# Kernel optimization log

Hardware: AMD Instinct MI355X
Metric: run time of the kernel (lower is better)

Reference implementation:

```python
import jax, jax.numpy as jnp
import numpy as np

B, S, E, H, L, D, G, V = 32, 256, 300, 256, 4000, 256, 512, 50000
LIN1, LIN2 = 512, 256  # linear_size


def _glorot(key, shape):
    fan_in, fan_out = shape[-1], shape[-2] if len(shape) > 1 else shape[-1]
    std = np.sqrt(2.0 / (fan_in + fan_out))
    return jax.random.normal(key, shape, dtype=jnp.float32) * std


def setup_inputs() -> dict:
    key = jax.random.key(0)
    ks = jax.random.split(key, 20)
    tokens = jax.random.randint(ks[0], (B, S), 1, V)  # avoid padding_idx=0
    emb_table = jax.random.normal(ks[1], (V, E), dtype=jnp.float32) * 0.1
    emb_table = emb_table.at[0].set(0.0)  # padding row
    # bidirectional LSTM (1 layer), torch gate order i,f,g,o
    w_ih_f = _glorot(ks[2], (4 * H, E));  w_hh_f = _glorot(ks[3], (4 * H, H))
    b_f = jnp.zeros((4 * H,), jnp.float32)
    w_ih_b = _glorot(ks[4], (4 * H, E));  w_hh_b = _glorot(ks[5], (4 * H, H))
    b_b = jnp.zeros((4 * H,), jnp.float32)
    # MLAttention: Linear(2H -> L, bias=False)
    attn_w = _glorot(ks[6], (L, 2 * H))
    # label graph branch
    label_emb = _glorot(ks[7], (L, D))
    adj_raw = (jax.random.uniform(ks[8], (L, L)) < 0.004).astype(jnp.float32)
    adj_raw = adj_raw + jnp.eye(L, dtype=jnp.float32)
    deg = jnp.sum(adj_raw, axis=1, keepdims=True)
    adj = adj_raw / deg  # row-normalized dense adjacency [L, L]
    gcn_w = _glorot(ks[9], (D, G));  gcn_b = jnp.zeros((G,), jnp.float32)
    # MLLinear([2H+G, 512, 256], 1)
    w1 = _glorot(ks[10], (2 * H + G, LIN1));  b1 = jnp.zeros((LIN1,), jnp.float32)
    w2 = _glorot(ks[11], (LIN1, LIN2));       b2 = jnp.zeros((LIN2,), jnp.float32)
    w_out = _glorot(ks[12], (LIN2, 1));       b_out = jnp.zeros((1,), jnp.float32)
    return dict(tokens=tokens, emb_table=emb_table,
                w_ih_f=w_ih_f, w_hh_f=w_hh_f, b_f=b_f,
                w_ih_b=w_ih_b, w_hh_b=w_hh_b, b_b=b_b,
                attn_w=attn_w, label_emb=label_emb, adj=adj,
                gcn_w=gcn_w, gcn_b=gcn_b,
                w1=w1, b1=b1, w2=w2, b2=b2, w_out=w_out, b_out=b_out)


def _lstm_dir(x_gates, w_hh, reverse):
    # x_gates: [B, S, 4H] precomputed input projections (+bias)
    def step(carry, xt):
        h, c = carry
        gates = xt + h @ w_hh.T
        i, f, g, o = jnp.split(gates, 4, axis=-1)
        c = jax.nn.sigmoid(f) * c + jax.nn.sigmoid(i) * jnp.tanh(g)
        h = jax.nn.sigmoid(o) * jnp.tanh(c)
        return (h, c), h
    b = x_gates.shape[0]
    init = (jnp.zeros((b, H), x_gates.dtype), jnp.zeros((b, H), x_gates.dtype))
    _, hs = jax.lax.scan(step, init, jnp.swapaxes(x_gates, 0, 1), reverse=reverse)
    return jnp.swapaxes(hs, 0, 1)  # [B, S, H]


def reference(tokens, emb_table, w_ih_f, w_hh_f, b_f, w_ih_b, w_hh_b, b_b,
              attn_w, label_emb, adj, gcn_w, gcn_b,
              w1, b1, w2, b2, w_out, b_out):
    masks = tokens != 0  # [B, S]
    emb_out = emb_table[tokens]  # [B, S, E]
    # bidirectional LSTM -> [B, S, 2H]
    gates_f = jnp.einsum('bse,ge->bsg', emb_out, w_ih_f) + b_f
    gates_b = jnp.einsum('bse,ge->bsg', emb_out, w_ih_b) + b_b
    rnn_out = jnp.concatenate([_lstm_dir(gates_f, w_hh_f, False),
                               _lstm_dir(gates_b, w_hh_b, True)], axis=-1)
    # MLAttention: per-label attention over sequence
    scores = jnp.einsum('bsh,lh->bls', rnn_out, attn_w)  # [B, L, S]
    scores = jnp.where(masks[:, None, :], scores, jnp.float32(-1e9))
    attn = jax.nn.softmax(scores, axis=-1)
    attn_out = jnp.einsum('bls,bsh->blh', attn, rnn_out)  # [B, L, 2H]
    # GCN over label graph: relu(A @ (X W) + b), single layer [D -> G]
    gcn_out = jax.nn.relu(adj @ (label_emb @ gcn_w) + gcn_b)  # [L, G]
    gcn_out = jnp.broadcast_to(gcn_out[None], (attn_out.shape[0], L, G))
    # concat fusion + MLLinear([2H+G, 512, 256], 1)
    x = jnp.concatenate([attn_out, gcn_out], axis=-1)  # [B, L, 2H+G]
    x = jax.nn.relu(x @ w1 + b1)
    x = jax.nn.relu(x @ w2 + b2)
    out = jnp.squeeze(x @ w_out + b_out, -1)  # [B, L]
    return out
```

## Files before the change

kernel.cpp:

```cpp
#include <hip/hip_runtime.h>
#include <hip/hip_bf16.h>
#include <math.h>


typedef __attribute__((ext_vector_type(8))) short bfrag;
typedef __attribute__((ext_vector_type(4))) float ffrag;

__device__ __forceinline__ ushort f2bf(float x) {
    union { float f; unsigned u; } c; c.f = x;
    const unsigned r = c.u + 0x7fffu + ((c.u >> 16) & 1u);
    return (ushort)(r >> 16);
}
__device__ __forceinline__ float bf2f(ushort h) {
    union { unsigned u; float f; } c; c.u = (unsigned)h << 16;
    return c.f;
}

template<bool BT, bool GATHER>
__global__ __launch_bounds__(256) void gemm_k(
    const float* __restrict__ A, const float* __restrict__ Bm, float* __restrict__ C,
    int M, int N, int K, int lda, int ldb, int ldc,
    long abs_, long bbs_, long cbs_,
    const int* __restrict__ tok,
    const float* __restrict__ bias,
    const float* __restrict__ addrow, int addmod, int ldadd,
    int do_relu)
{
    const int tid = threadIdx.x;
    const int tx = tid & 15;
    const int ty = tid >> 4;
    const int n0 = blockIdx.x * 128;
    const int m0 = blockIdx.y * 64;
    const int z  = blockIdx.z;
    A  += (size_t)z * abs_;
    Bm += (size_t)z * bbs_;
    C  += (size_t)z * cbs_;

    __shared__ float As[16][68];
    __shared__ float Bs[16][132];

    float acc[4][8];
#pragma unroll
    for (int i = 0; i < 4; ++i)
#pragma unroll
        for (int j = 0; j < 8; ++j) acc[i][j] = 0.f;

    const int ksteps = (K + 15) / 16;
    for (int kt = 0; kt < ksteps; ++kt) {
        const int k0 = kt * 16;
#pragma unroll
        for (int j = 0; j < 4; ++j) {
            int e  = tid + j * 256;
            int kk = e & 15;
            int m  = e >> 4;
            int gm = m0 + m, gk = k0 + kk;
            float v = 0.f;
            if (gm < M && gk < K) {
                size_t rb;
                if (GATHER) rb = (size_t)tok[gm] * lda;
                else        rb = (size_t)gm * lda;
                v = A[rb + gk];
            }
            As[kk][m] = v;
        }
#pragma unroll
        for (int j = 0; j < 8; ++j) {
            int e = tid + j * 256;
            if (BT) {
                int kk = e & 15;
                int n  = e >> 4;
                int gn = n0 + n, gk = k0 + kk;
                Bs[kk][n] = (gn < N && gk < K) ? Bm[(size_t)gn * ldb + gk] : 0.f;
            } else {
                int n  = e & 127;
                int kk = e >> 7;
                int gn = n0 + n, gk = k0 + kk;
                Bs[kk][n] = (gn < N && gk < K) ? Bm[(size_t)gk * ldb + gn] : 0.f;
            }
        }
        __syncthreads();
#pragma unroll
        for (int kk = 0; kk < 16; ++kk) {
            const float4 av  = *(const float4*)&As[kk][ty * 4];
            const float4 b0v = *(const float4*)&Bs[kk][tx * 8];
            const float4 b1v = *(const float4*)&Bs[kk][tx * 8 + 4];
            const float a_[4] = {av.x, av.y, av.z, av.w};
            const float b_[8] = {b0v.x, b0v.y, b0v.z, b0v.w, b1v.x, b1v.y, b1v.z, b1v.w};
#pragma unroll
            for (int i = 0; i < 4; ++i)
#pragma unroll
                for (int j = 0; j < 8; ++j) acc[i][j] = fmaf(a_[i], b_[j], acc[i][j]);
        }
        __syncthreads();
    }

#pragma unroll
    for (int i = 0; i < 4; ++i) {
        const int gm = m0 + ty * 4 + i;
        if (gm >= M) continue;
        const float* addp = addrow ? (addrow + (size_t)(gm % addmod) * ldadd) : nullptr;
#pragma unroll
        for (int j = 0; j < 8; ++j) {
            const int gn = n0 + tx * 8 + j;
            if (gn >= N) continue;
            float v = acc[i][j];
            if (bias) v += bias[gn];
            if (addp) v += addp[gn];
            if (do_relu) v = fmaxf(v, 0.f);
            C[(size_t)gm * ldc + gn] = v;
        }
    }
}

template<bool BIAS, bool ADDROW, bool RELU, bool OUTF, bool OUTS>
__global__ __launch_bounds__(256) void mgemm_k(
    const ushort* __restrict__ A, const ushort* __restrict__ B,
    float* __restrict__ Cf, ushort* __restrict__ Cs,
    int M, int N, int K, int lda, int ldb, int ldc, int ldcs,
    long abs_, long bbs_, long cbs_, long csbs_,
    const float* __restrict__ bias,
    const float* __restrict__ addrow, int addmod, int ldadd)
{
    const int tid = threadIdx.x;
    const int ln = tid & 63;
    const int wv = tid >> 6;
    const int wm = wv >> 1, wn = wv & 1;
    const int m0 = blockIdx.x * 128, n0 = blockIdx.y * 128;
    const int z = blockIdx.z;
    A += (size_t)z * abs_;
    B += (size_t)z * bbs_;

    __shared__ ushort Ah[128 * 40], Al[128 * 40], Bh[128 * 40], Bl[128 * 40];

    ffrag acc[4][4];
#pragma unroll
    for (int i = 0; i < 4; ++i)
#pragma unroll
        for (int j = 0; j < 4; ++j) acc[i][j] = ffrag{0.f, 0.f, 0.f, 0.f};

    const int sr = tid >> 1;
    const int sk = (tid & 1) * 16;
    const int am = min(m0 + sr, M - 1);
    const int bn = n0 + sr;
    const int fr = ln & 15;
    const int fk = (ln >> 4) * 8;

    const ushort* arow = A + (size_t)am * lda;
    const ushort* brow = B + (size_t)bn * ldb;

    for (int k0 = 0; k0 < K; k0 += 32) {
        const ushort* ap = arow + k0 + sk;
        const ushort* bp = brow + k0 + sk;
        const bfrag ah0 = *(const bfrag*)ap;
        const bfrag ah1 = *(const bfrag*)(ap + 8);
        const bfrag al0 = *(const bfrag*)(ap + K);
        const bfrag al1 = *(const bfrag*)(ap + K + 8);
        const bfrag bh0 = *(const bfrag*)bp;
        const bfrag bh1 = *(const bfrag*)(bp + 8);
        const bfrag bl0 = *(const bfrag*)(bp + K);
        const bfrag bl1 = *(const bfrag*)(bp + K + 8);
        __syncthreads();
        *(bfrag*)&Ah[sr * 40 + sk] = ah0;  *(bfrag*)&Ah[sr * 40 + sk + 8] = ah1;
        *(bfrag*)&Al[sr * 40 + sk] = al0;  *(bfrag*)&Al[sr * 40 + sk + 8] = al1;
        *(bfrag*)&Bh[sr * 40 + sk] = bh0;  *(bfrag*)&Bh[sr * 40 + sk + 8] = bh1;
        *(bfrag*)&Bl[sr * 40 + sk] = bl0;  *(bfrag*)&Bl[sr * 40 + sk + 8] = bl1;
        __syncthreads();
        bfrag afh[4], afl[4], bfh[4], bfl[4];
#pragma unroll
        for (int i = 0; i < 4; ++i) {
            const int ar = (wm * 64 + i * 16 + fr) * 40 + fk;
            const int br = (wn * 64 + i * 16 + fr) * 40 + fk;
            afh[i] = *(const bfrag*)&Ah[ar];
            afl[i] = *(const bfrag*)&Al[ar];
            bfh[i] = *(const bfrag*)&Bh[br];
            bfl[i] = *(const bfrag*)&Bl[br];
        }
#pragma unroll
        for (int i = 0; i < 4; ++i)
#pragma unroll
            for (int j = 0; j < 4; ++j) {
                acc[i][j] = __builtin_amdgcn_mfma_f32_16x16x32_bf16(afh[i], bfh[j], acc[i][j], 0, 0, 0);
                acc[i][j] = __builtin_amdgcn_mfma_f32_16x16x32_bf16(afh[i], bfl[j], acc[i][j], 0, 0, 0);
                acc[i][j] = __builtin_amdgcn_mfma_f32_16x16x32_bf16(afl[i], bfh[j], acc[i][j], 0, 0, 0);
            }
    }

#pragma unroll
    for (int i = 0; i < 4; ++i) {
#pragma unroll
        for (int rg = 0; rg < 4; ++rg) {
            const int gm = m0 + wm * 64 + i * 16 + (ln >> 4) * 4 + rg;
            if (gm >= M) continue;
            const float* addp = ADDROW ? (addrow + (size_t)(gm % addmod) * ldadd) : nullptr;
#pragma unroll
            for (int j = 0; j < 4; ++j) {
                const int gn = n0 + wn * 64 + j * 16 + fr;
                float v = acc[i][j][rg];
                if (BIAS) v += bias[gn];
                if (ADDROW) v += addp[gn];
                if (RELU) v = fmaxf(v, 0.f);
                if (OUTF) Cf[(size_t)z * cbs_ + (size_t)gm * ldc + gn] = v;
                if (OUTS) {
                    const ushort h = f2bf(v);
                    const ushort l = f2bf(v - bf2f(h));
                    ushort* cp = Cs + (size_t)z * csbs_ + (size_t)gm * ldcs;
                    cp[gn] = h;
                    cp[N + gn] = l;
                }
            }
        }
    }
}

__global__ void gsplit_k(const float* __restrict__ src, const int* __restrict__ tok,
                         ushort* __restrict__ outp, int K, int Kpad)
{
    const int r = blockIdx.x;
    const float* s = src + (size_t)(tok ? tok[r] : r) * K;
    ushort* o = outp + (size_t)r * 2 * Kpad;
    for (int k = threadIdx.x; k < Kpad; k += blockDim.x) {
        const float x = (k < K) ? s[k] : 0.f;
        const ushort h = f2bf(x);
        const ushort l = f2bf(x - bf2f(h));
        o[k] = h;
        o[Kpad + k] = l;
    }
}

__global__ void split_k(const float* __restrict__ in, ushort* __restrict__ outp,
                        int rows, int K)
{
    const int i = blockIdx.x * 256 + threadIdx.x;
    if (i >= rows * K) return;
    const int r = i / K, k = i - r * K;
    const float x = in[i];
    const ushort h = f2bf(x);
    const ushort l = f2bf(x - bf2f(h));
    ushort* o = outp + (size_t)r * 2 * K;
    o[k] = h;
    o[K + k] = l;
}

__global__ __launch_bounds__(256) void tsplit_k(
    const float* __restrict__ in, ushort* __restrict__ outp,
    int R, int C, int ldin, long ibs, long obs)
{
    __shared__ float t[64][65];
    const int c0 = blockIdx.x * 64, r0 = blockIdx.y * 64;
    in   += (size_t)blockIdx.z * ibs;
    outp += (size_t)blockIdx.z * obs;
    const int tx = threadIdx.x & 15, ty = threadIdx.x >> 4;
#pragma unroll
    for (int i = 0; i < 4; ++i) {
        const int r = ty * 4 + i;
        const float4 v = *(const float4*)&in[(size_t)(r0 + r) * ldin + c0 + tx * 4];
        t[tx * 4 + 0][r] = v.x;
        t[tx * 4 + 1][r] = v.y;
        t[tx * 4 + 2][r] = v.z;
        t[tx * 4 + 3][r] = v.w;
    }
    __syncthreads();
    const int R2 = 2 * R;
#pragma unroll
    for (int i = 0; i < 4; ++i) {
        const int c = ty * 4 + i;
        ushort h[4], l[4];
#pragma unroll
        for (int k2 = 0; k2 < 4; ++k2) {
            const float x = t[c][tx * 4 + k2];
            h[k2] = f2bf(x);
            l[k2] = f2bf(x - bf2f(h[k2]));
        }
        uint2 hw, lw;
        hw.x = (unsigned)h[0] | ((unsigned)h[1] << 16);
        hw.y = (unsigned)h[2] | ((unsigned)h[3] << 16);
        lw.x = (unsigned)l[0] | ((unsigned)l[1] << 16);
        lw.y = (unsigned)l[2] | ((unsigned)l[3] << 16);
        *(uint2*)&outp[(size_t)(c0 + c) * R2 + r0 + tx * 4] = hw;
        *(uint2*)&outp[(size_t)(c0 + c) * R2 + R + r0 + tx * 4] = lw;
    }
}

__global__ __launch_bounds__(1024) void lstm_reg_k(
    const float* __restrict__ gxf, const float* __restrict__ gxb,
    const float* __restrict__ whf, const float* __restrict__ whb,
    float* __restrict__ rnn, float* hbuf, int* stamp)
{
    const int p = blockIdx.x;
    const int q = blockIdx.y;
    const int b = p >> 1, dir = p & 1;
    const float* xg = dir ? gxb : gxf;
    const float* W  = dir ? whb : whf;
    const int tid = threadIdx.x;
    const int wv = tid >> 6, lane = tid & 63;
    const int ul = lane >> 4;
    const int u  = wv * 4 + ul;
    const int gt = (lane >> 2) & 3;
    const int ks = lane & 3;
    const int grow = gt * 256 + q * 64 + u;

    float4 w[16];
    {
        const float4* wp = (const float4*)(W + (size_t)grow * 256 + ks * 64);
#pragma unroll
        for (int i = 0; i < 16; ++i) w[i] = wp[i];
    }

    __shared__ float h_lds[4 * 68];
    __shared__ float xg_lds[256];

    float* hb0 = hbuf + (size_t)p * 256;
    float* hb1 = hbuf + (size_t)(64 + p) * 256;
    int* sp = stamp + p * 16;

    const size_t xgb = (size_t)b * 256;
    const int g2 = (tid >> 6) * 256 + q * 64 + (tid & 63);
    float c = 0.f;
    float xg_cur = 0.f;
    if (tid < 256) xg_cur = xg[(xgb + (dir ? 255 : 0)) * 1024 + g2];

    for (int st = 0; st < 256; ++st) {
        const int ts = dir ? 255 - st : st;
        if (st > 0 && tid == 0) {
            while (true) {
                int s0 = __hip_atomic_load(&sp[0], __ATOMIC_RELAXED, __HIP_MEMORY_SCOPE_AGENT);
                int s1 = __hip_atomic_load(&sp[1], __ATOMIC_RELAXED, __HIP_MEMORY_SCOPE_AGENT);
                int s2 = __hip_atomic_load(&sp[2], __ATOMIC_RELAXED, __HIP_MEMORY_SCOPE_AGENT);
                int s3 = __hip_atomic_load(&sp[3], __ATOMIC_RELAXED, __HIP_MEMORY_SCOPE_AGENT);
                if (min(min(s0, s1), min(s2, s3)) >= st) break;
            }
        }
        __syncthreads();
        if (tid < 256) {
            float hv = 0.f;
            if (st > 0) {
                const float* src = (st & 1) ? hb0 : hb1;
                hv = __hip_atomic_load(&src[tid], __ATOMIC_RELAXED, __HIP_MEMORY_SCOPE_AGENT);
            }
            h_lds[(tid >> 6) * 68 + (tid & 63)] = hv;
            xg_lds[tid] = xg_cur;
        }
        __syncthreads();
        float acc = 0.f;
        {
            const float4* hp = (const float4*)&h_lds[ks * 68];
#pragma unroll
            for (int i = 0; i < 16; ++i) {
                const float4 hv = hp[i];
                acc = fmaf(w[i].x, hv.x, acc);
                acc = fmaf(w[i].y, hv.y, acc);
                acc = fmaf(w[i].z, hv.z, acc);
                acc = fmaf(w[i].w, hv.w, acc);
            }
        }
        acc += __shfl_xor(acc, 1);
        acc += __shfl_xor(acc, 2);
        const float g = acc + xg_lds[gt * 64 + u];
        const int base = ul * 16;
        const float gi = __shfl(g, base);
        const float gf = __shfl(g, base + 4);
        const float gg = __shfl(g, base + 8);
        const float go = __shfl(g, base + 12);
        if ((lane & 15) == 0) {
            const float si = 1.f / (1.f + __expf(-gi));
            const float sf = 1.f / (1.f + __expf(-gf));
            const float so = 1.f / (1.f + __expf(-go));
            const float tg = 1.f - 2.f / (__expf(2.f * gg) + 1.f);
            c = sf * c + si * tg;
            const float tc = 1.f - 2.f / (__expf(2.f * c) + 1.f);
            const float hn = so * tc;
            float* dst = (st & 1) ? hb1 : hb0;
            __hip_atomic_store(&dst[q * 64 + u], hn, __ATOMIC_RELAXED, __HIP_MEMORY_SCOPE_AGENT);
            rnn[(xgb + ts) * 512 + (size_t)dir * 256 + q * 64 + u] = hn;
        }
        __syncthreads();
        if (tid == 0) {
            __hip_atomic_store(&sp[q], st + 1, __ATOMIC_RELAXED, __HIP_MEMORY_SCOPE_AGENT);
        }
        if (tid < 256 && st < 255) {
            const int tsn = dir ? 254 - st : st + 1;
            xg_cur = xg[(xgb + tsn) * 1024 + g2];
        }
    }
}

__global__ void init_cnt_k(int* stamp) {
    const int i = blockIdx.x * blockDim.x + threadIdx.x;
    if (i < 1024) stamp[i] = 0;
}

__global__ __launch_bounds__(256) void softmax_split_k(
    float* __restrict__ sc, const int* __restrict__ tokens, int b0)
{
    const int bb = blockIdx.y;
    const int l  = blockIdx.x * 4 + (threadIdx.x >> 6);
    const int lane = threadIdx.x & 63;
    float* row = sc + ((size_t)bb * 4000 + l) * 256;
    const int* tk = tokens + (size_t)(b0 + bb) * 256;
    float4 v = *(const float4*)&row[lane * 4];
    const int4 tv = *(const int4*)&tk[lane * 4];
    if (tv.x == 0) v.x = -1e9f;
    if (tv.y == 0) v.y = -1e9f;
    if (tv.z == 0) v.z = -1e9f;
    if (tv.w == 0) v.w = -1e9f;
    float mx = fmaxf(fmaxf(v.x, v.y), fmaxf(v.z, v.w));
    for (int o = 32; o > 0; o >>= 1) mx = fmaxf(mx, __shfl_xor(mx, o));
    v.x = __expf(v.x - mx); v.y = __expf(v.y - mx);
    v.z = __expf(v.z - mx); v.w = __expf(v.w - mx);
    float s = v.x + v.y + v.z + v.w;
    for (int o = 32; o > 0; o >>= 1) s += __shfl_xor(s, o);
    const float inv = 1.f / s;
    const float p0 = v.x * inv, p1 = v.y * inv, p2 = v.z * inv, p3 = v.w * inv;
    const ushort h0 = f2bf(p0), h1 = f2bf(p1), h2 = f2bf(p2), h3 = f2bf(p3);
    const ushort l0 = f2bf(p0 - bf2f(h0)), l1 = f2bf(p1 - bf2f(h1));
    const ushort l2 = f2bf(p2 - bf2f(h2)), l3 = f2bf(p3 - bf2f(h3));
    ushort* orow = (ushort*)row;
    uint2 hw, lw;
    hw.x = (unsigned)h0 | ((unsigned)h1 << 16);
    hw.y = (unsigned)h2 | ((unsigned)h3 << 16);
    lw.x = (unsigned)l0 | ((unsigned)l1 << 16);
    lw.y = (unsigned)l2 | ((unsigned)l3 << 16);
    *(uint2*)&orow[lane * 4] = hw;
    *(uint2*)&orow[256 + lane * 4] = lw;
}

__global__ __launch_bounds__(256) void spmm_k(
    const float* __restrict__ adj, const float* __restrict__ tmp,
    const float* __restrict__ bias, float* __restrict__ outp)
{
    const int l = blockIdx.x;
    __shared__ int   idxs[4][256];
    __shared__ float vals[4][256];
    __shared__ int   cnts[4];
    const int t = threadIdx.x;
    const int w = t >> 6, lane = t & 63;
    const float* arow = adj + (size_t)l * 4000;
    int cnt = 0;
    for (int r = 0; r < 16; ++r) {
        const int o = r * 64 + lane;
        const int j = w * 1000 + o;
        const float a = (o < 1000) ? arow[j] : 0.f;
        const unsigned long long mk = __ballot(a != 0.f);
        if (a != 0.f) {
            const int pos = cnt + __popcll(mk & ((1ull << lane) - 1ull));
            if (pos < 256) { idxs[w][pos] = j; vals[w][pos] = a; }
        }
        cnt += __popcll(mk);
    }
    if (lane == 0) cnts[w] = min(cnt, 256);
    __syncthreads();
    const int c0 = t * 2;
    float a0 = 0.f, a1 = 0.f;
    for (int ww = 0; ww < 4; ++ww) {
        const int n = cnts[ww];
        for (int e = 0; e < n; ++e) {
            const float a = vals[ww][e];
            const float2 tv = *(const float2*)&tmp[(size_t)idxs[ww][e] * 512 + c0];
            a0 = fmaf(a, tv.x, a0);
            a1 = fmaf(a, tv.y, a1);
        }
    }
    float2 res;
    res.x = fmaxf(a0 + bias[c0], 0.f);
    res.y = fmaxf(a1 + bias[c0 + 1], 0.f);
    *(float2*)&outp[(size_t)l * 512 + c0] = res;
}

__global__ __launch_bounds__(256) void out_k(
    const float* __restrict__ x2, const float* __restrict__ w_out,
    const float* __restrict__ b_out, float* __restrict__ outp, int b0)
{
    const int r = blockIdx.x * 4 + (threadIdx.x >> 6);
    const int lane = threadIdx.x & 63;
    const float4 xv = *(const float4*)&x2[(size_t)r * 256 + lane * 4];
    const float4 wv = *(const float4*)&w_out[lane * 4];
    float s = xv.x * wv.x + xv.y * wv.y + xv.z * wv.z + xv.w * wv.w;
    for (int o = 32; o > 0; o >>= 1) s += __shfl_xor(s, o);
    if (lane == 0) {
        const int bb = r / 4000, l = r - bb * 4000;
        outp[(size_t)(b0 + bb) * 4000 + l] = s + b_out[0];
    }
}

extern "C" void kernel_launch(void* const* d_in, const int* in_sizes, int n_in,
                              void* d_out, int out_size, void* d_ws, size_t ws_size,
                              hipStream_t stream)
{
    const int*   tokens    = (const int*)  d_in[0];
    const float* emb       = (const float*)d_in[1];
    const float* w_ih_f    = (const float*)d_in[2];
    const float* w_hh_f    = (const float*)d_in[3];
    const float* b_f       = (const float*)d_in[4];
    const float* w_ih_b    = (const float*)d_in[5];
    const float* w_hh_b    = (const float*)d_in[6];
    const float* b_b       = (const float*)d_in[7];
    const float* attn_w    = (const float*)d_in[8];
    const float* label_emb = (const float*)d_in[9];
    const float* adj       = (const float*)d_in[10];
    const float* gcn_w     = (const float*)d_in[11];
    const float* gcn_b     = (const float*)d_in[12];
    const float* w1        = (const float*)d_in[13];
    const float* b1        = (const float*)d_in[14];
    const float* w2        = (const float*)d_in[15];
    const float* b2        = (const float*)d_in[16];
    const float* w_out     = (const float*)d_in[17];
    const float* b_out     = (const float*)d_in[18];
    float* outp = (float*)d_out;
    float* wsf  = (float*)d_ws;

    const size_t off_gf  = 0;
    const size_t off_gb  = 8388608;
    const size_t off_rnn = 16777216;
    const size_t off_tmp = 20971520;
    const size_t off_go  = 23019520;
    const size_t off_ctr = 25067520;
    const size_t base_end = 27115520;
    const size_t S_sz = 10829824;
    const size_t have = ws_size / 4;
    int NB; size_t offS, offC;
    if      (have >= base_end + S_sz + 4ul * 5120000) { NB = 4; offS = base_end; offC = base_end + S_sz; }
    else if (have >= base_end + S_sz + 2ul * 5120000) { NB = 2; offS = base_end; offC = base_end + S_sz; }
    else if (have >= base_end + S_sz)                 { NB = 2; offS = base_end; offC = off_gf; }
    else { NB = 1; offS = off_gf; offC = off_gf + S_sz; }

    float* gates_f = wsf + off_gf;
    float* gates_b = wsf + off_gb;
    float* rnn     = wsf + off_rnn;
    float* gcn_tmp = wsf + off_tmp;
    float* gcn_out = wsf + off_go;
    float* contrib = wsf + off_ctr;
    float* hbuf    = wsf + off_tmp;
    int*   stamp   = (int*)(wsf + off_tmp + 32768);

    const size_t off_esp = (offS == off_gf) ? off_rnn : offS;
    ushort* esplit  = (ushort*)(wsf + off_esp);
    ushort* wsplitf = esplit + (size_t)8192 * 640;
    ushort* wsplitb = wsplitf + (size_t)1024 * 640;

    ushort* attn_ws16 = (ushort*)(wsf + offS);
    ushort* w1t16     = (ushort*)(wsf + offS + 2048000);
    ushort* w2t16     = (ushort*)(wsf + offS + 2310144);
    ushort* rnn_nt16  = (ushort*)(wsf + offS + 2441216);
    ushort* rnnT16    = (ushort*)(wsf + offS + 6635520);

    float*  scoresb = wsf + offC;
    ushort* attn16  = (ushort*)(wsf + offC + (size_t)NB * 1024000);
    ushort* x116    = (ushort*)(wsf + offC + (size_t)NB * 1024000 + (size_t)NB * 2048000);
    float*  x2b     = scoresb;

    init_cnt_k<<<4, 256, 0, stream>>>(stamp);

    gsplit_k<<<8192, 256, 0, stream>>>(emb, tokens, esplit, 300, 320);
    gsplit_k<<<1024, 256, 0, stream>>>(w_ih_f, nullptr, wsplitf, 300, 320);
    gsplit_k<<<1024, 256, 0, stream>>>(w_ih_b, nullptr, wsplitb, 300, 320);
    mgemm_k<true, false, false, true, false><<<dim3(64, 8, 1), 256, 0, stream>>>(
        esplit, wsplitf, gates_f, nullptr,
        8192, 1024, 320, 640, 640, 1024, 0,
        0L, 0L, 0L, 0L, b_f, nullptr, 1, 0);
    mgemm_k<true, false, false, true, false><<<dim3(64, 8, 1), 256, 0, stream>>>(
        esplit, wsplitb, gates_b, nullptr,
        8192, 1024, 320, 640, 640, 1024, 0,
        0L, 0L, 0L, 0L, b_b, nullptr, 1, 0);

    lstm_reg_k<<<dim3(64, 4), 1024, 0, stream>>>(
        gates_f, gates_b, w_hh_f, w_hh_b, rnn, hbuf, stamp);

    split_k<<<16384, 256, 0, stream>>>(rnn, rnn_nt16, 8192, 512);
    tsplit_k<<<dim3(8, 4, 32), 256, 0, stream>>>(rnn, rnnT16, 256, 512, 512, 131072, 262144);
    split_k<<<8000, 256, 0, stream>>>(attn_w, attn_ws16, 4000, 512);
    tsplit_k<<<dim3(8, 8, 1), 256, 0, stream>>>(w1, w1t16, 512, 512, 512, 0, 0);
    tsplit_k<<<dim3(4, 8, 1), 256, 0, stream>>>(w2, w2t16, 512, 256, 256, 0, 0);

    gemm_k<false, false><<<dim3(4, 63, 1), 256, 0, stream>>>(
        label_emb, gcn_w, gcn_tmp, 4000, 512, 256, 256, 512, 512,
        0, 0, 0, nullptr, nullptr, nullptr, 1, 0, 0);
    spmm_k<<<dim3(4000), 256, 0, stream>>>(adj, gcn_tmp, gcn_b, gcn_out);
    gemm_k<false, false><<<dim3(4, 63, 1), 256, 0, stream>>>(
        gcn_out, w1 + (size_t)512 * 512, contrib, 4000, 512, 512, 512, 512, 512,
        0, 0, 0, nullptr, b1, nullptr, 1, 0, 0);

    for (int b0 = 0; b0 < 32; b0 += NB) {
        const int nb = (32 - b0 < NB) ? (32 - b0) : NB;
        mgemm_k<false, false, false, true, false><<<dim3(32, 2, nb), 256, 0, stream>>>(
            attn_ws16, rnn_nt16 + (size_t)b0 * 262144, scoresb, nullptr,
            4000, 256, 512, 1024, 1024, 256, 0,
            0L, 262144L, 1024000L, 0L, nullptr, nullptr, 1, 0);
        softmax_split_k<<<dim3(1000, nb), 256, 0, stream>>>(scoresb, tokens, b0);
        mgemm_k<false, false, false, false, true><<<dim3(32, 4, nb), 256, 0, stream>>>(
            (const ushort*)scoresb, rnnT16 + (size_t)b0 * 262144, nullptr, attn16,
            4000, 512, 256, 512, 512, 0, 1024,
            2048000L, 262144L, 0L, 4096000L, nullptr, nullptr, 1, 0);
        mgemm_k<false, true, true, false, true><<<dim3((nb * 4000 + 127) / 128, 4, 1), 256, 0, stream>>>(
            attn16, w1t16, nullptr, x116,
            nb * 4000, 512, 512, 1024, 1024, 0, 1024,
            0L, 0L, 0L, 0L, nullptr, contrib, 4000, 512);
        mgemm_k<true, false, true, true, false><<<dim3((nb * 4000 + 127) / 128, 2, 1), 256, 0, stream>>>(
            x116, w2t16, x2b, nullptr,
            nb * 4000, 256, 512, 1024, 1024, 256, 0,
            0L, 0L, 0L, 0L, b2, nullptr, 1, 0);
        out_k<<<dim3(nb * 1000), 256, 0, stream>>>(x2b, w_out, b_out, outp, b0);
    }
}
```

Before: 2.028 ms.

## Prefetch GEMM tiles, redistribute LSTM gate math across lanes, widen batch chunking

The split-bf16 GEMM now loads the next K-slice from global memory into registers while the current tile is consumed from LDS, and it streams B fragments per column to lower register pressure. The LSTM kernel remaps lanes so that each group of four lanes holds the four gates of one unit. Every lane computes the activations redundantly, which removes the serialized single-lane activation math and the extra shuffles, at the cost of a padded LDS layout for the gate inputs. The workspace tiering now allows larger batch chunks (up to 32) when the workspace is big enough, which cuts the number of attention-stage launches.

```diff
diff --git a/kernel.cpp b/kernel.cpp
--- a/kernel.cpp
+++ b/kernel.cpp
@@ -145,44 +145,53 @@
     const int fr = ln & 15;
     const int fk = (ln >> 4) * 8;
 
-    const ushort* arow = A + (size_t)am * lda;
-    const ushort* brow = B + (size_t)bn * ldb;
+    const ushort* arow = A + (size_t)am * lda + sk;
+    const ushort* brow = B + (size_t)bn * ldb + sk;
+
+    bfrag ah0, ah1, al0, al1, bh0, bh1, bl0, bl1;
+    {
+        const ushort* ap = arow;
+        const ushort* bp = brow;
+        ah0 = *(const bfrag*)ap;       ah1 = *(const bfrag*)(ap + 8);
+        al0 = *(const bfrag*)(ap + K); al1 = *(const bfrag*)(ap + K + 8);
+        bh0 = *(const bfrag*)bp;       bh1 = *(const bfrag*)(bp + 8);
+        bl0 = *(const bfrag*)(bp + K); bl1 = *(const bfrag*)(bp + K + 8);
+    }
 
     for (int k0 = 0; k0 < K; k0 += 32) {
-        const ushort* ap = arow + k0 + sk;
-        const ushort* bp = brow + k0 + sk;
-        const bfrag ah0 = *(const bfrag*)ap;
-        const bfrag ah1 = *(const bfrag*)(ap + 8);
-        const bfrag al0 = *(const bfrag*)(ap + K);
-        const bfrag al1 = *(const bfrag*)(ap + K + 8);
-        const bfrag bh0 = *(const bfrag*)bp;
-        const bfrag bh1 = *(const bfrag*)(bp + 8);
-        const bfrag bl0 = *(const bfrag*)(bp + K);
-        const bfrag bl1 = *(const bfrag*)(bp + K + 8);
         __syncthreads();
         *(bfrag*)&Ah[sr * 40 + sk] = ah0;  *(bfrag*)&Ah[sr * 40 + sk + 8] = ah1;
         *(bfrag*)&Al[sr * 40 + sk] = al0;  *(bfrag*)&Al[sr * 40 + sk + 8] = al1;
         *(bfrag*)&Bh[sr * 40 + sk] = bh0;  *(bfrag*)&Bh[sr * 40 + sk + 8] = bh1;
         *(bfrag*)&Bl[sr * 40 + sk] = bl0;  *(bfrag*)&Bl[sr * 40 + sk + 8] = bl1;
         __syncthreads();
-        bfrag afh[4], afl[4], bfh[4], bfl[4];
+        if (k0 + 32 < K) {
+            const ushort* ap = arow + k0 + 32;
+            const ushort* bp = brow + k0 + 32;
+            ah0 = *(const bfrag*)ap;       ah1 = *(const bfrag*)(ap + 8);
+            al0 = *(const bfrag*)(ap + K); al1 = *(const bfrag*)(ap + K + 8);
+            bh0 = *(const bfrag*)bp;       bh1 = *(const bfrag*)(bp + 8);
+            bl0 = *(const bfrag*)(bp + K); bl1 = *(const bfrag*)(bp + K + 8);
+        }
+        bfrag afh[4], afl[4];
 #pragma unroll
         for (int i = 0; i < 4; ++i) {
             const int ar = (wm * 64 + i * 16 + fr) * 40 + fk;
-            const int br = (wn * 64 + i * 16 + fr) * 40 + fk;
             afh[i] = *(const bfrag*)&Ah[ar];
             afl[i] = *(const bfrag*)&Al[ar];
-            bfh[i] = *(const bfrag*)&Bh[br];
-            bfl[i] = *(const bfrag*)&Bl[br];
-        }
-#pragma unroll
-        for (int i = 0; i < 4; ++i)
-#pragma unroll
-            for (int j = 0; j < 4; ++j) {
-                acc[i][j] = __builtin_amdgcn_mfma_f32_16x16x32_bf16(afh[i], bfh[j], acc[i][j], 0, 0, 0);
-                acc[i][j] = __builtin_amdgcn_mfma_f32_16x16x32_bf16(afh[i], bfl[j], acc[i][j], 0, 0, 0);
-                acc[i][j] = __builtin_amdgcn_mfma_f32_16x16x32_bf16(afl[i], bfh[j], acc[i][j], 0, 0, 0);
-            }
+        }
+#pragma unroll
+        for (int j = 0; j < 4; ++j) {
+            const int br = (wn * 64 + j * 16 + fr) * 40 + fk;
+            const bfrag bfh = *(const bfrag*)&Bh[br];
+            const bfrag bfl = *(const bfrag*)&Bl[br];
+#pragma unroll
+            for (int i = 0; i < 4; ++i) {
+                acc[i][j] = __builtin_amdgcn_mfma_f32_16x16x32_bf16(afh[i], bfh, acc[i][j], 0, 0, 0);
+                acc[i][j] = __builtin_amdgcn_mfma_f32_16x16x32_bf16(afh[i], bfl, acc[i][j], 0, 0, 0);
+                acc[i][j] = __builtin_amdgcn_mfma_f32_16x16x32_bf16(afl[i], bfh, acc[i][j], 0, 0, 0);
+            }
+        }
     }
 
 #pragma unroll
@@ -294,9 +303,9 @@
     const int tid = threadIdx.x;
     const int wv = tid >> 6, lane = tid & 63;
     const int ul = lane >> 4;
+    const int ks = (lane >> 2) & 3;
+    const int gt = lane & 3;
     const int u  = wv * 4 + ul;
-    const int gt = (lane >> 2) & 3;
-    const int ks = lane & 3;
     const int grow = gt * 256 + q * 64 + u;
 
     float4 w[16];
@@ -307,7 +316,7 @@
     }
 
     __shared__ float h_lds[4 * 68];
-    __shared__ float xg_lds[256];
+    __shared__ float xg_lds[320];
 
     float* hb0 = hbuf + (size_t)p * 256;
     float* hb1 = hbuf + (size_t)(64 + p) * 256;
@@ -338,7 +347,7 @@
                 hv = __hip_atomic_load(&src[tid], __ATOMIC_RELAXED, __HIP_MEMORY_SCOPE_AGENT);
             }
             h_lds[(tid >> 6) * 68 + (tid & 63)] = hv;
-            xg_lds[tid] = xg_cur;
+            xg_lds[(tid & 63) * 5 + (tid >> 6)] = xg_cur;
         }
         __syncthreads();
         float acc = 0.f;
@@ -353,22 +362,24 @@
                 acc = fmaf(w[i].w, hv.w, acc);
             }
         }
-        acc += __shfl_xor(acc, 1);
-        acc += __shfl_xor(acc, 2);
-        const float g = acc + xg_lds[gt * 64 + u];
-        const int base = ul * 16;
-        const float gi = __shfl(g, base);
-        const float gf = __shfl(g, base + 4);
-        const float gg = __shfl(g, base + 8);
-        const float go = __shfl(g, base + 12);
+        acc += __shfl_xor(acc, 4);
+        acc += __shfl_xor(acc, 8);
+        const float g = acc + xg_lds[u * 5 + gt];
+        const float t1 = __shfl_xor(g, 1);
+        const float t2 = __shfl_xor(g, 2);
+        const float t3 = __shfl_xor(t1, 2);
+        const float g0 = (gt == 0) ? g : (gt == 1) ? t1 : (gt == 2) ? t2 : t3;
+        const float g1 = (gt == 1) ? g : (gt == 0) ? t1 : (gt == 3) ? t2 : t3;
+        const float g2v = (gt == 2) ? g : (gt == 3) ? t1 : (gt == 0) ? t2 : t3;
+        const float g3v = (gt == 3) ? g : (gt == 2) ? t1 : (gt == 1) ? t2 : t3;
+        const float si = 1.f / (1.f + __expf(-g0));
+        const float sf = 1.f / (1.f + __expf(-g1));
+        const float so = 1.f / (1.f + __expf(-g3v));
+        const float tg = 1.f - 2.f / (__expf(2.f * g2v) + 1.f);
+        c = sf * c + si * tg;
+        const float tc = 1.f - 2.f / (__expf(2.f * c) + 1.f);
+        const float hn = so * tc;
         if ((lane & 15) == 0) {
-            const float si = 1.f / (1.f + __expf(-gi));
-            const float sf = 1.f / (1.f + __expf(-gf));
-            const float so = 1.f / (1.f + __expf(-go));
-            const float tg = 1.f - 2.f / (__expf(2.f * gg) + 1.f);
-            c = sf * c + si * tg;
-            const float tc = 1.f - 2.f / (__expf(2.f * c) + 1.f);
-            const float hn = so * tc;
             float* dst = (st & 1) ? hb1 : hb0;
             __hip_atomic_store(&dst[q * 64 + u], hn, __ATOMIC_RELAXED, __HIP_MEMORY_SCOPE_AGENT);
             rnn[(xgb + ts) * 512 + (size_t)dir * 256 + q * 64 + u] = hn;
@@ -517,11 +528,17 @@
     const size_t base_end = 27115520;
     const size_t S_sz = 10829824;
     const size_t have = ws_size / 4;
-    int NB; size_t offS, offC;
-    if      (have >= base_end + S_sz + 4ul * 5120000) { NB = 4; offS = base_end; offC = base_end + S_sz; }
-    else if (have >= base_end + S_sz + 2ul * 5120000) { NB = 2; offS = base_end; offC = base_end + S_sz; }
-    else if (have >= base_end + S_sz)                 { NB = 2; offS = base_end; offC = off_gf; }
-    else { NB = 1; offS = off_gf; offC = off_gf + S_sz; }
+    int NB = 1; size_t offS = off_gf, offC = off_gf + S_sz;
+    {
+        const int tiers[6] = {32, 16, 8, 4, 2, 0};
+        bool found = false;
+        for (int t = 0; tiers[t]; ++t) {
+            if (have >= base_end + S_sz + (size_t)tiers[t] * 5120000) {
+                NB = tiers[t]; offS = base_end; offC = base_end + S_sz; found = true; break;
+            }
+        }
+        if (!found && have >= base_end + S_sz) { NB = 2; offS = base_end; offC = off_gf; }
+    }
 
     float* gates_f = wsf + off_gf;
     float* gates_b = wsf + off_gb;
```

Result: faster. 1.967 ms (-3.0%).
